# Performance work log

Hardware: AMD Instinct MI355X
Metric: run time of the kernel (lower is better)

## Reference

```python
import jax, jax.numpy as jnp
import numpy as np

N = 50000   # nodes per graph slot
E = 800000  # edges per graph slot
F = 768     # num_node_features
H = 256     # hidden_channels
G = 4       # max_graphs
B = 32      # graphs in batch
C1 = H * (G + 1)  # concat_channels = 1280


def setup_inputs() -> dict:
    key = jax.random.key(0)
    ks = iter(jax.random.split(key, 32))
    inp = {}
    for g in range(G):
        inp[f"x_g{g}"] = jax.random.normal(next(ks), (N, F), jnp.float32)
        inp[f"ei_g{g}"] = jax.random.randint(next(ks), (2, E), 0, N, jnp.int32)
        inp[f"batch_g{g}"] = jnp.sort(jax.random.randint(next(ks), (N,), 0, B, jnp.int32))
    inp["x_code"] = jax.random.normal(next(ks), (B, F), jnp.float32)
    s = 0.02
    inp["W1"] = jax.random.normal(next(ks), (F, H), jnp.float32) * s
    inp["b1"] = jnp.zeros((H,), jnp.float32)
    inp["W2"] = jax.random.normal(next(ks), (H, H), jnp.float32) * s
    inp["b2"] = jnp.zeros((H,), jnp.float32)
    inp["W3"] = jax.random.normal(next(ks), (H, H), jnp.float32) * s
    inp["b3"] = jnp.zeros((H,), jnp.float32)
    inp["Wc"] = jax.random.normal(next(ks), (F, H), jnp.float32) * s
    inp["bc"] = jnp.zeros((H,), jnp.float32)
    inp["Wl1"] = jax.random.normal(next(ks), (C1, C1 // 2), jnp.float32) * s
    inp["bl1"] = jnp.zeros((C1 // 2,), jnp.float32)
    inp["Wl2"] = jax.random.normal(next(ks), (C1 // 2, 2), jnp.float32) * s
    inp["bl2"] = jnp.zeros((2,), jnp.float32)
    return inp


def gcn_conv(x, W, b, src, dst):
    n = x.shape[0]
    h = x @ W                                   # [n, H]
    loops = jnp.arange(n, dtype=src.dtype)
    s = jnp.concatenate([src, loops])
    d = jnp.concatenate([dst, loops])
    deg = jax.ops.segment_sum(jnp.ones(s.shape[0], x.dtype), d, num_segments=n)
    dinv = jnp.where(deg > 0, jax.lax.rsqrt(deg), 0.0)
    norm = dinv[s] * dinv[d]                    # [E+n]
    return jax.ops.segment_sum(h[s] * norm[:, None], d, num_segments=n) + b


def global_mean_pool(x, batch, num_graphs):
    s = jax.ops.segment_sum(x, batch, num_segments=num_graphs)
    c = jax.ops.segment_sum(jnp.ones(x.shape[0], x.dtype), batch, num_segments=num_graphs)
    return s / jnp.maximum(c, 1.0)[:, None]


def reference(x_g0, x_g1, x_g2, x_g3, ei_g0, ei_g1, ei_g2, ei_g3,
              batch_g0, batch_g1, batch_g2, batch_g3, x_code,
              W1, b1, W2, b2, W3, b3, Wc, bc, Wl1, bl1, Wl2, bl2):
    nb = x_code.shape[0]
    pooled = []
    for x, ei, bi in zip((x_g0, x_g1, x_g2, x_g3),
                         (ei_g0, ei_g1, ei_g2, ei_g3),
                         (batch_g0, batch_g1, batch_g2, batch_g3)):
        h = jax.nn.relu(gcn_conv(x, W1, b1, ei[0], ei[1]))
        h = jax.nn.relu(gcn_conv(h, W2, b2, ei[0], ei[1]))
        h = gcn_conv(h, W3, b3, ei[0], ei[1])
        pooled.append(global_mean_pool(h, bi, nb))      # [B, H]
    xc = jax.nn.relu(x_code @ Wc + bc)                  # [B, H]
    pooled.append(xc)
    x_concat = jnp.concatenate(pooled, axis=1)          # [B, H*(G+1)]
    h = jax.nn.relu(x_concat @ Wl1 + bl1)
    # dropout p=0.2 with training=False -> identity
    logits = h @ Wl2 + bl2                              # [B, 2]
    return logits
```

## Files before the change

kernel.cpp:

```cpp
#include <hip/hip_runtime.h>
#include <hip/hip_bf16.h>

#define N_NODES 50000
#define N_EDGES 800000
#define F_IN    768
#define H_DIM   256
#define N_B     32
#define N_G     4
#define C1      1280
#define C2      640

typedef unsigned short u16;
typedef unsigned int u32;
typedef __bf16 bf16x8 __attribute__((ext_vector_type(8)));
typedef float f32x4 __attribute__((ext_vector_type(4)));

__device__ inline u16 f2b(float f) {
    u32 u = __builtin_bit_cast(u32, f);
    u += 0x7fffu + ((u >> 16) & 1u);
    return (u16)(u >> 16);
}
__device__ inline float b2f(u16 h) {
    u32 u = ((u32)h) << 16;
    return __builtin_bit_cast(float, u);
}
__device__ inline u32 pack2(float a, float b) {
    return (u32)f2b(a) | ((u32)f2b(b) << 16);
}


__global__ void count_deg_kernel(const int* __restrict__ dst, int* __restrict__ deg, int n_edges) {
    int e = blockIdx.x * blockDim.x + threadIdx.x;
    if (e < n_edges) atomicAdd(&deg[dst[e]], 1);
}

__global__ __launch_bounds__(1024) void scan1_kernel(const int* __restrict__ deg,
                                                     int* __restrict__ bsum, int n) {
    __shared__ int ws[16];
    int tid = threadIdx.x, lane = tid & 63, wid = tid >> 6;
    int i = blockIdx.x * 1024 + tid;
    int x = (i < n) ? deg[i] : 0;
#pragma unroll
    for (int off = 32; off; off >>= 1) x += __shfl_xor(x, off, 64);
    if (lane == 0) ws[wid] = x;
    __syncthreads();
    if (tid == 0) {
        int s = 0;
#pragma unroll
        for (int w = 0; w < 16; w++) s += ws[w];
        bsum[blockIdx.x] = s;
    }
}

__global__ __launch_bounds__(64) void scan2_kernel(int* __restrict__ bsum, int nb,
                                                   int* __restrict__ row_start, int n) {
    int lane = threadIdx.x;
    int x = (lane < nb) ? bsum[lane] : 0;
    int v = x;
#pragma unroll
    for (int off = 1; off < 64; off <<= 1) {
        int t = __shfl_up(v, off, 64);
        if (lane >= off) v += t;
    }
    if (lane < nb) bsum[lane] = v - x;
    if (lane == 63) row_start[n] = v;
}

__global__ __launch_bounds__(1024) void scan3_kernel(const int* __restrict__ deg,
                                                     const int* __restrict__ bsum,
                                                     int* __restrict__ row_start,
                                                     int* __restrict__ cursor,
                                                     float* __restrict__ dinv, int n) {
    __shared__ int ws[16];
    int tid = threadIdx.x, lane = tid & 63, wid = tid >> 6;
    int i = blockIdx.x * 1024 + tid;
    int x = (i < n) ? deg[i] : 0;
    int v = x;
#pragma unroll
    for (int off = 1; off < 64; off <<= 1) {
        int t = __shfl_up(v, off, 64);
        if (lane >= off) v += t;
    }
    if (lane == 63) ws[wid] = v;
    __syncthreads();
    if (wid == 0) {
        int s = (lane < 16) ? ws[lane] : 0;
#pragma unroll
        for (int off = 1; off < 16; off <<= 1) {
            int t = __shfl_up(s, off, 64);
            if (lane >= off) s += t;
        }
        if (lane < 16) ws[lane] = s;
    }
    __syncthreads();
    if (i < n) {
        int excl = bsum[blockIdx.x] + (wid ? ws[wid - 1] : 0) + (v - x);
        row_start[i] = excl;
        cursor[i] = excl;
        dinv[i] = rsqrtf((float)(x + 1));
    }
}

__global__ void fill_csr_kernel(const int* __restrict__ src, const int* __restrict__ dst,
                                int* __restrict__ cursor, int* __restrict__ csr_src, int n_edges) {
    int e = blockIdx.x * blockDim.x + threadIdx.x;
    if (e < n_edges) {
        int d = dst[e];
        int pos = atomicAdd(&cursor[d], 1);
        csr_src[pos] = src[e];
    }
}


__global__ void prep_w_kernel(const float* __restrict__ W, u16* __restrict__ Wt, int K) {
    int idx = blockIdx.x * blockDim.x + threadIdx.x;
    if (idx >= K * 256) return;
    int k = idx >> 8, n = idx & 255;
    Wt[(size_t)n * K + k] = f2b(W[idx]);
}


__global__ __launch_bounds__(256) void gemm_mfma_kernel(const void* __restrict__ Aptr, int a_fp32,
                                                        const u16* __restrict__ Wt,
                                                        const float* __restrict__ dinv,
                                                        u16* __restrict__ Cout, int n, int K) {
    __shared__ u16 As[64 * 32] __attribute__((aligned(16)));
    __shared__ u16 Bs[256 * 32] __attribute__((aligned(16)));
    int tid = threadIdx.x;
    int row0 = blockIdx.x * 64;
    int wid = tid >> 6, lane = tid & 63;
    int mlane = lane & 15, kg = lane >> 4;

    int ra = tid >> 2;
    int koffa = (tid & 3) << 3;
    int rga = row0 + ra; if (rga >= n) rga = n - 1;

    f32x4 acc[4][4];
#pragma unroll
    for (int a = 0; a < 4; a++)
#pragma unroll
        for (int b = 0; b < 4; b++)
#pragma unroll
            for (int c = 0; c < 4; c++) acc[a][b][c] = 0.f;

    for (int k0 = 0; k0 < K; k0 += 32) {
        if (a_fp32) {
            const float* A = (const float*)Aptr;
            const float* srcp = A + (size_t)rga * K + k0 + koffa;
            float4 f0 = *(const float4*)srcp;
            float4 f1 = *(const float4*)(srcp + 4);
            int4 v;
            v.x = (int)pack2(f0.x, f0.y);
            v.y = (int)pack2(f0.z, f0.w);
            v.z = (int)pack2(f1.x, f1.y);
            v.w = (int)pack2(f1.z, f1.w);
            *(int4*)&As[ra * 32 + koffa] = v;
        } else {
            const u16* A = (const u16*)Aptr;
            *(int4*)&As[ra * 32 + koffa] = *(const int4*)(A + (size_t)rga * K + k0 + koffa);
        }
#pragma unroll
        for (int it = 0; it < 4; it++) {
            int c = tid + it * 256;
            int r = c >> 2;
            int koff = (c & 3) << 3;
            *(int4*)&Bs[r * 32 + koff] = *(const int4*)(Wt + (size_t)r * K + k0 + koff);
        }
        __syncthreads();
        bf16x8 af[4], bfv[4];
#pragma unroll
        for (int mi = 0; mi < 4; mi++)
            af[mi] = *(const bf16x8*)&As[(mi * 16 + mlane) * 32 + kg * 8];
#pragma unroll
        for (int ni = 0; ni < 4; ni++)
            bfv[ni] = *(const bf16x8*)&Bs[(wid * 64 + ni * 16 + mlane) * 32 + kg * 8];
#pragma unroll
        for (int mi = 0; mi < 4; mi++)
#pragma unroll
            for (int ni = 0; ni < 4; ni++)
                acc[mi][ni] = __builtin_amdgcn_mfma_f32_16x16x32_bf16(af[mi], bfv[ni], acc[mi][ni], 0, 0, 0);
        __syncthreads();
    }
#pragma unroll
    for (int mi = 0; mi < 4; mi++) {
        int rbase = row0 + mi * 16 + kg * 4;
#pragma unroll
        for (int r = 0; r < 4; r++) {
            int row = rbase + r;
            if (row < n) {
                float s = dinv[row];
#pragma unroll
                for (int ni = 0; ni < 4; ni++) {
                    int col = wid * 64 + ni * 16 + mlane;
                    Cout[(size_t)row * H_DIM + col] = f2b(acc[mi][ni][r] * s);
                }
            }
        }
    }
}


__global__ __launch_bounds__(64) void aggregate_kernel(const u16* __restrict__ Ht,
                                                       const int* __restrict__ row_start,
                                                       const int* __restrict__ csr_src,
                                                       const float* __restrict__ dinv,
                                                       const float* __restrict__ bias,
                                                       u16* __restrict__ out, int do_relu) {
    int i = blockIdx.x;
    int c4 = threadIdx.x << 2;
    ushort4 sv = *(const ushort4*)(Ht + (size_t)i * H_DIM + c4);
    float a0 = b2f(sv.x), a1 = b2f(sv.y), a2 = b2f(sv.z), a3 = b2f(sv.w);
    int s = row_start[i], e = row_start[i + 1];
    for (int p = s; p < e; p++) {
        int j = csr_src[p];
        ushort4 v = *(const ushort4*)(Ht + (size_t)j * H_DIM + c4);
        a0 += b2f(v.x); a1 += b2f(v.y); a2 += b2f(v.z); a3 += b2f(v.w);
    }
    float di = dinv[i];
    float4 b = *(const float4*)(bias + c4);
    float o0 = a0 * di + b.x, o1 = a1 * di + b.y, o2 = a2 * di + b.z, o3 = a3 * di + b.w;
    if (do_relu) {
        o0 = fmaxf(o0, 0.f); o1 = fmaxf(o1, 0.f);
        o2 = fmaxf(o2, 0.f); o3 = fmaxf(o3, 0.f);
    }
    ushort4 ov = make_ushort4(f2b(o0), f2b(o1), f2b(o2), f2b(o3));
    *(ushort4*)(out + (size_t)i * H_DIM + c4) = ov;
}


__global__ __launch_bounds__(256) void pool_kernel(const u16* __restrict__ h3,
                                                   const int* __restrict__ batch,
                                                   float* __restrict__ concat, int g) {
    int tid = threadIdx.x;
    int per = (N_NODES + (int)gridDim.x - 1) / (int)gridDim.x;
    int start = blockIdx.x * per;
    int end = min(N_NODES, start + per);
    if (start >= end) return;
    float acc = 0.f;
    int cur = batch[start];
    for (int i = start; i < end; i++) {
        int b = batch[i];
        if (b != cur) {
            atomicAdd(&concat[cur * C1 + g * H_DIM + tid], acc);
            acc = 0.f;
            cur = b;
        }
        acc += b2f(h3[(size_t)i * H_DIM + tid]);
    }
    atomicAdd(&concat[cur * C1 + g * H_DIM + tid], acc);
}

__global__ __launch_bounds__(64) void count_kernel(const int* __restrict__ batch,
                                                   float* __restrict__ cnt, int g) {
    __shared__ int bound[N_B + 1];
    int t = threadIdx.x;
    if (t <= N_B) {
        int lo = 0, hi = N_NODES;
        while (lo < hi) {
            int mid = (lo + hi) >> 1;
            if (batch[mid] < t) lo = mid + 1; else hi = mid;
        }
        bound[t] = lo;
    }
    __syncthreads();
    if (t < N_B) cnt[g * N_B + t] = (float)(bound[t + 1] - bound[t]);
}

__global__ void pool_div_kernel(float* __restrict__ concat, const float* __restrict__ cnt) {
    int idx = blockIdx.x * blockDim.x + threadIdx.x;
    int g = idx >> 13;
    int r = idx & 8191;
    int b = r >> 8;
    int f = r & 255;
    float c = fmaxf(cnt[g * N_B + b], 1.f);
    concat[b * C1 + g * H_DIM + f] /= c;
}


__global__ void xc_kernel(const float* __restrict__ x_code, const float* __restrict__ Wc,
                          const float* __restrict__ bc, float* __restrict__ concat) {
    int idx = blockIdx.x * blockDim.x + threadIdx.x;
    int b = idx >> 8, c = idx & 255;
    float acc = bc[c];
    for (int k = 0; k < F_IN; k++) acc += x_code[b * F_IN + k] * Wc[k * H_DIM + c];
    concat[b * C1 + 4 * H_DIM + c] = fmaxf(acc, 0.f);
}

__global__ void mlp1_kernel(const float* __restrict__ concat, const float* __restrict__ Wl1,
                            const float* __restrict__ bl1, float* __restrict__ hmid) {
    int idx = blockIdx.x * blockDim.x + threadIdx.x;
    int b = idx / C2, c = idx % C2;
    float acc = bl1[c];
    for (int k = 0; k < C1; k++) acc += concat[b * C1 + k] * Wl1[k * C2 + c];
    hmid[b * C2 + c] = fmaxf(acc, 0.f);
}

__global__ void mlp2_kernel(const float* __restrict__ hmid, const float* __restrict__ Wl2,
                            const float* __restrict__ bl2, float* __restrict__ out) {
    int idx = threadIdx.x;
    if (idx < N_B * 2) {
        int b = idx >> 1, c = idx & 1;
        float acc = bl2[c];
        for (int k = 0; k < C2; k++) acc += hmid[b * C2 + k] * Wl2[k * 2 + c];
        out[b * 2 + c] = acc;
    }
}


extern "C" void kernel_launch(void* const* d_in, const int* in_sizes, int n_in,
                              void* d_out, int out_size, void* d_ws, size_t ws_size,
                              hipStream_t stream) {
    const float* x_g[N_G];
    const int* ei[N_G];
    const int* batch[N_G];
    for (int g = 0; g < N_G; g++) {
        x_g[g]   = (const float*)d_in[3 * g + 0];
        ei[g]    = (const int*)d_in[3 * g + 1];
        batch[g] = (const int*)d_in[3 * g + 2];
    }
    const float* x_code = (const float*)d_in[12];
    const float* W1 = (const float*)d_in[13];
    const float* b1 = (const float*)d_in[14];
    const float* W2 = (const float*)d_in[15];
    const float* b2 = (const float*)d_in[16];
    const float* W3 = (const float*)d_in[17];
    const float* b3 = (const float*)d_in[18];
    const float* Wc = (const float*)d_in[19];
    const float* bc = (const float*)d_in[20];
    const float* Wl1 = (const float*)d_in[21];
    const float* bl1 = (const float*)d_in[22];
    const float* Wl2 = (const float*)d_in[23];
    const float* bl2 = (const float*)d_in[24];
    float* out = (float*)d_out;

    char* p = (char*)d_ws;
    auto alloc = [&](size_t bytes) -> void* {
        void* q = (void*)p;
        p += (bytes + 255) & ~(size_t)255;
        return q;
    };
    u16*   bufA      = (u16*)alloc((size_t)N_NODES * H_DIM * 2);
    u16*   bufB      = (u16*)alloc((size_t)N_NODES * H_DIM * 2);
    u16*   Wt1       = (u16*)alloc((size_t)H_DIM * F_IN * 2);
    u16*   Wt2       = (u16*)alloc((size_t)H_DIM * H_DIM * 2);
    u16*   Wt3       = (u16*)alloc((size_t)H_DIM * H_DIM * 2);
    int*   row_start = (int*)alloc((size_t)(N_NODES + 1) * 4);
    int*   cursor    = (int*)alloc((size_t)N_NODES * 4);
    int*   csr_src   = (int*)alloc((size_t)N_EDGES * 4);
    int*   deg       = (int*)alloc((size_t)N_NODES * 4);
    float* dinv      = (float*)alloc((size_t)N_NODES * 4);
    float* concat    = (float*)alloc((size_t)N_B * C1 * 4);
    float* cnt       = (float*)alloc((size_t)N_G * N_B * 4);
    float* hmid      = (float*)alloc((size_t)N_B * C2 * 4);
    int*   bsum      = (int*)alloc((size_t)64 * 4);

    hipMemsetAsync(concat, 0, (size_t)N_B * C1 * 4, stream);

    prep_w_kernel<<<(F_IN * 256 + 255) / 256, 256, 0, stream>>>(W1, Wt1, F_IN);
    prep_w_kernel<<<(H_DIM * 256 + 255) / 256, 256, 0, stream>>>(W2, Wt2, H_DIM);
    prep_w_kernel<<<(H_DIM * 256 + 255) / 256, 256, 0, stream>>>(W3, Wt3, H_DIM);

    dim3 gemm_grid((N_NODES + 63) / 64);
    int nb_scan = (N_NODES + 1023) / 1024;

    for (int g = 0; g < N_G; g++) {
        const int* src = ei[g];
        const int* dst = ei[g] + N_EDGES;
        hipMemsetAsync(deg, 0, (size_t)N_NODES * 4, stream);
        count_deg_kernel<<<(N_EDGES + 255) / 256, 256, 0, stream>>>(dst, deg, N_EDGES);
        scan1_kernel<<<nb_scan, 1024, 0, stream>>>(deg, bsum, N_NODES);
        scan2_kernel<<<1, 64, 0, stream>>>(bsum, nb_scan, row_start, N_NODES);
        scan3_kernel<<<nb_scan, 1024, 0, stream>>>(deg, bsum, row_start, cursor, dinv, N_NODES);
        fill_csr_kernel<<<(N_EDGES + 255) / 256, 256, 0, stream>>>(src, dst, cursor, csr_src, N_EDGES);

        gemm_mfma_kernel<<<gemm_grid, 256, 0, stream>>>(x_g[g], 1, Wt1, dinv, bufA, N_NODES, F_IN);
        aggregate_kernel<<<N_NODES, 64, 0, stream>>>(bufA, row_start, csr_src, dinv, b1, bufB, 1);
        gemm_mfma_kernel<<<gemm_grid, 256, 0, stream>>>(bufB, 0, Wt2, dinv, bufA, N_NODES, H_DIM);
        aggregate_kernel<<<N_NODES, 64, 0, stream>>>(bufA, row_start, csr_src, dinv, b2, bufB, 1);
        gemm_mfma_kernel<<<gemm_grid, 256, 0, stream>>>(bufB, 0, Wt3, dinv, bufA, N_NODES, H_DIM);
        aggregate_kernel<<<N_NODES, 64, 0, stream>>>(bufA, row_start, csr_src, dinv, b3, bufB, 0);

        pool_kernel<<<2048, 256, 0, stream>>>(bufB, batch[g], concat, g);
        count_kernel<<<1, 64, 0, stream>>>(batch[g], cnt, g);
    }

    pool_div_kernel<<<(N_G * N_B * H_DIM) / 256, 256, 0, stream>>>(concat, cnt);
    xc_kernel<<<(N_B * H_DIM) / 256, 256, 0, stream>>>(x_code, Wc, bc, concat);
    mlp1_kernel<<<(N_B * C2) / 256, 256, 0, stream>>>(concat, Wl1, bl1, hmid);
    mlp2_kernel<<<1, 64, 0, stream>>>(hmid, Wl2, bl2, out);
}
```

Baseline: 2.277 ms.

## Double-buffer GEMM LDS tiles with register prefetch, pad LDS, batch aggregate nodes

The MFMA GEMM now stages A and B tiles through registers into double-buffered shared memory, so global loads for the next two k-steps overlap the MFMA work and one barrier per step is dropped. Shared-memory rows are padded to 40 elements to reduce bank conflicts on the fragment reads. The aggregation kernel handles four nodes per 256-thread block instead of one node per 64-thread block, which cuts block-launch overhead. Shared memory use per GEMM block roughly doubles, which may lower occupancy.

```diff
diff --git a/kernel.cpp b/kernel.cpp
--- a/kernel.cpp
+++ b/kernel.cpp
@@ -9,6 +9,7 @@
 #define N_G     4
 #define C1      1280
 #define C2      640
+#define LDA     40
 
 typedef unsigned short u16;
 typedef unsigned int u32;
@@ -124,8 +125,8 @@
                                                         const u16* __restrict__ Wt,
                                                         const float* __restrict__ dinv,
                                                         u16* __restrict__ Cout, int n, int K) {
-    __shared__ u16 As[64 * 32] __attribute__((aligned(16)));
-    __shared__ u16 Bs[256 * 32] __attribute__((aligned(16)));
+    __shared__ u16 As[2 * 64 * LDA] __attribute__((aligned(16)));
+    __shared__ u16 Bs[2 * 256 * LDA] __attribute__((aligned(16)));
     int tid = threadIdx.x;
     int row0 = blockIdx.x * 64;
     int wid = tid >> 6, lane = tid & 63;
@@ -134,6 +135,8 @@
     int ra = tid >> 2;
     int koffa = (tid & 3) << 3;
     int rga = row0 + ra; if (rga >= n) rga = n - 1;
+    const float* Af = (const float*)Aptr;
+    const u16*  Ab = (const u16*)Aptr;
 
     f32x4 acc[4][4];
 #pragma unroll
@@ -143,43 +146,64 @@
 #pragma unroll
             for (int c = 0; c < 4; c++) acc[a][b][c] = 0.f;
 
-    for (int k0 = 0; k0 < K; k0 += 32) {
+    int nk = K >> 5;
+    int4 stA, stB0, stB1, stB2, stB3;
+
+    auto loadA = [&](int k0, int4& d) {
         if (a_fp32) {
-            const float* A = (const float*)Aptr;
-            const float* srcp = A + (size_t)rga * K + k0 + koffa;
-            float4 f0 = *(const float4*)srcp;
-            float4 f1 = *(const float4*)(srcp + 4);
-            int4 v;
-            v.x = (int)pack2(f0.x, f0.y);
-            v.y = (int)pack2(f0.z, f0.w);
-            v.z = (int)pack2(f1.x, f1.y);
-            v.w = (int)pack2(f1.z, f1.w);
-            *(int4*)&As[ra * 32 + koffa] = v;
+            const float* s = Af + (size_t)rga * K + k0 + koffa;
+            float4 f0 = *(const float4*)s;
+            float4 f1 = *(const float4*)(s + 4);
+            d.x = (int)pack2(f0.x, f0.y);
+            d.y = (int)pack2(f0.z, f0.w);
+            d.z = (int)pack2(f1.x, f1.y);
+            d.w = (int)pack2(f1.z, f1.w);
         } else {
-            const u16* A = (const u16*)Aptr;
-            *(int4*)&As[ra * 32 + koffa] = *(const int4*)(A + (size_t)rga * K + k0 + koffa);
-        }
-#pragma unroll
-        for (int it = 0; it < 4; it++) {
-            int c = tid + it * 256;
-            int r = c >> 2;
-            int koff = (c & 3) << 3;
-            *(int4*)&Bs[r * 32 + koff] = *(const int4*)(Wt + (size_t)r * K + k0 + koff);
-        }
-        __syncthreads();
+            d = *(const int4*)(Ab + (size_t)rga * K + k0 + koffa);
+        }
+    };
+    auto loadB = [&](int k0) {
+        stB0 = *(const int4*)(Wt + (size_t)(ra +   0) * K + k0 + koffa);
+        stB1 = *(const int4*)(Wt + (size_t)(ra +  64) * K + k0 + koffa);
+        stB2 = *(const int4*)(Wt + (size_t)(ra + 128) * K + k0 + koffa);
+        stB3 = *(const int4*)(Wt + (size_t)(ra + 192) * K + k0 + koffa);
+    };
+    auto writeStage = [&](int buf) {
+        *(int4*)&As[buf * (64 * LDA) + ra * LDA + koffa] = stA;
+        u16* bb = &Bs[buf * (256 * LDA)];
+        *(int4*)&bb[(ra +   0) * LDA + koffa] = stB0;
+        *(int4*)&bb[(ra +  64) * LDA + koffa] = stB1;
+        *(int4*)&bb[(ra + 128) * LDA + koffa] = stB2;
+        *(int4*)&bb[(ra + 192) * LDA + koffa] = stB3;
+    };
+
+    loadA(0, stA); loadB(0);
+    writeStage(0);
+    if (nk > 1) { loadA(32, stA); loadB(32); }
+    __syncthreads();
+
+    int cur = 0;
+    for (int t = 0; t < nk; t++) {
+        const u16* ab = &As[cur * (64 * LDA)];
+        const u16* bb = &Bs[cur * (256 * LDA)];
         bf16x8 af[4], bfv[4];
 #pragma unroll
         for (int mi = 0; mi < 4; mi++)
-            af[mi] = *(const bf16x8*)&As[(mi * 16 + mlane) * 32 + kg * 8];
+            af[mi] = *(const bf16x8*)&ab[(mi * 16 + mlane) * LDA + kg * 8];
 #pragma unroll
         for (int ni = 0; ni < 4; ni++)
-            bfv[ni] = *(const bf16x8*)&Bs[(wid * 64 + ni * 16 + mlane) * 32 + kg * 8];
+            bfv[ni] = *(const bf16x8*)&bb[(wid * 64 + ni * 16 + mlane) * LDA + kg * 8];
+        if (t + 1 < nk) {
+            writeStage(cur ^ 1);
+            if (t + 2 < nk) { loadA((t + 2) << 5, stA); loadB((t + 2) << 5); }
+        }
 #pragma unroll
         for (int mi = 0; mi < 4; mi++)
 #pragma unroll
             for (int ni = 0; ni < 4; ni++)
                 acc[mi][ni] = __builtin_amdgcn_mfma_f32_16x16x32_bf16(af[mi], bfv[ni], acc[mi][ni], 0, 0, 0);
         __syncthreads();
+        cur ^= 1;
     }
 #pragma unroll
     for (int mi = 0; mi < 4; mi++) {
@@ -200,14 +224,15 @@
 }
 
 
-__global__ __launch_bounds__(64) void aggregate_kernel(const u16* __restrict__ Ht,
-                                                       const int* __restrict__ row_start,
-                                                       const int* __restrict__ csr_src,
-                                                       const float* __restrict__ dinv,
-                                                       const float* __restrict__ bias,
-                                                       u16* __restrict__ out, int do_relu) {
-    int i = blockIdx.x;
-    int c4 = threadIdx.x << 2;
+__global__ __launch_bounds__(256) void aggregate_kernel(const u16* __restrict__ Ht,
+                                                        const int* __restrict__ row_start,
+                                                        const int* __restrict__ csr_src,
+                                                        const float* __restrict__ dinv,
+                                                        const float* __restrict__ bias,
+                                                        u16* __restrict__ out, int do_relu) {
+    int i = blockIdx.x * 4 + (threadIdx.x >> 6);
+    if (i >= N_NODES) return;
+    int c4 = (threadIdx.x & 63) << 2;
     ushort4 sv = *(const ushort4*)(Ht + (size_t)i * H_DIM + c4);
     float a0 = b2f(sv.x), a1 = b2f(sv.y), a2 = b2f(sv.z), a3 = b2f(sv.w);
     int s = row_start[i], e = row_start[i + 1];
@@ -361,6 +386,7 @@
     prep_w_kernel<<<(H_DIM * 256 + 255) / 256, 256, 0, stream>>>(W3, Wt3, H_DIM);
 
     dim3 gemm_grid((N_NODES + 63) / 64);
+    dim3 agg_grid((N_NODES + 3) / 4);
     int nb_scan = (N_NODES + 1023) / 1024;
 
     for (int g = 0; g < N_G; g++) {
@@ -374,11 +400,11 @@
         fill_csr_kernel<<<(N_EDGES + 255) / 256, 256, 0, stream>>>(src, dst, cursor, csr_src, N_EDGES);
 
         gemm_mfma_kernel<<<gemm_grid, 256, 0, stream>>>(x_g[g], 1, Wt1, dinv, bufA, N_NODES, F_IN);
-        aggregate_kernel<<<N_NODES, 64, 0, stream>>>(bufA, row_start, csr_src, dinv, b1, bufB, 1);
+        aggregate_kernel<<<agg_grid, 256, 0, stream>>>(bufA, row_start, csr_src, dinv, b1, bufB, 1);
         gemm_mfma_kernel<<<gemm_grid, 256, 0, stream>>>(bufB, 0, Wt2, dinv, bufA, N_NODES, H_DIM);
-        aggregate_kernel<<<N_NODES, 64, 0, stream>>>(bufA, row_start, csr_src, dinv, b2, bufB, 1);
+        aggregate_kernel<<<agg_grid, 256, 0, stream>>>(bufA, row_start, csr_src, dinv, b2, bufB, 1);
         gemm_mfma_kernel<<<gemm_grid, 256, 0, stream>>>(bufB, 0, Wt3, dinv, bufA, N_NODES, H_DIM);
-        aggregate_kernel<<<N_NODES, 64, 0, stream>>>(bufA, row_start, csr_src, dinv, b3, bufB, 0);
+        aggregate_kernel<<<agg_grid, 256, 0, stream>>>(bufA, row_start, csr_src, dinv, b3, bufB, 0);
 
         pool_kernel<<<2048, 256, 0, stream>>>(bufB, batch[g], concat, g);
         count_kernel<<<1, 64, 0, stream>>>(batch[g], cnt, g);
```

Result: slower. 2.556 ms (+12.3%).

## Software-pipeline GEMM with double-buffered LDS, direct B register loads, swizzle

Applied to the files above, without the earlier changes.

Rewrites the node-feature GEMM as a template on K and input type, so the inner loop is specialised at compile time. The A tile is double-buffered in LDS with an XOR swizzle to cut bank conflicts. Global loads for the next K-step are issued before the current step's MFMAs, overlapping memory latency with compute. The weight operand is loaded straight from global memory into registers, skipping LDS staging. In exchange, register pressure rises and each wave re-reads the weights from cache instead of sharing them through LDS.

```diff
diff --git a/kernel.cpp b/kernel.cpp
--- a/kernel.cpp
+++ b/kernel.cpp
@@ -120,20 +120,26 @@
 }
 
 
-__global__ __launch_bounds__(256) void gemm_mfma_kernel(const void* __restrict__ Aptr, int a_fp32,
+template<int K, bool AFP32>
+__global__ __launch_bounds__(256) void gemm_mfma_kernel(const void* __restrict__ Aptr,
                                                         const u16* __restrict__ Wt,
                                                         const float* __restrict__ dinv,
-                                                        u16* __restrict__ Cout, int n, int K) {
-    __shared__ u16 As[64 * 32] __attribute__((aligned(16)));
-    __shared__ u16 Bs[256 * 32] __attribute__((aligned(16)));
+                                                        u16* __restrict__ Cout, int n) {
+    constexpr int NK = K / 32;
+    __shared__ u16 As[2 * 2048] __attribute__((aligned(16)));
     int tid = threadIdx.x;
     int row0 = blockIdx.x * 64;
     int wid = tid >> 6, lane = tid & 63;
     int mlane = lane & 15, kg = lane >> 4;
 
     int ra = tid >> 2;
-    int koffa = (tid & 3) << 3;
+    int qa = tid & 3;
     int rga = row0 + ra; if (rga >= n) rga = n - 1;
+    const float* Af = (const float*)Aptr;
+    const u16*  Ab = (const u16*)Aptr;
+    int awr = (ra * 32 + qa * 8) ^ (((ra >> 1) & 3) << 3);
+
+    const u16* wtb = Wt + (size_t)(wid * 64 + mlane) * K + kg * 8;
 
     f32x4 acc[4][4];
 #pragma unroll
@@ -143,44 +149,69 @@
 #pragma unroll
             for (int c = 0; c < 4; c++) acc[a][b][c] = 0.f;
 
-    for (int k0 = 0; k0 < K; k0 += 32) {
-        if (a_fp32) {
-            const float* A = (const float*)Aptr;
-            const float* srcp = A + (size_t)rga * K + k0 + koffa;
-            float4 f0 = *(const float4*)srcp;
-            float4 f1 = *(const float4*)(srcp + 4);
-            int4 v;
-            v.x = (int)pack2(f0.x, f0.y);
-            v.y = (int)pack2(f0.z, f0.w);
-            v.z = (int)pack2(f1.x, f1.y);
-            v.w = (int)pack2(f1.z, f1.w);
-            *(int4*)&As[ra * 32 + koffa] = v;
+    float4 rF0, rF1; int4 rA;
+    auto loadA = [&](int s) {
+        int k0 = (s < NK ? s : NK - 1) * 32;
+        if constexpr (AFP32) {
+            const float* sp = Af + (size_t)rga * K + k0 + qa * 8;
+            rF0 = *(const float4*)sp;
+            rF1 = *(const float4*)(sp + 4);
         } else {
-            const u16* A = (const u16*)Aptr;
-            *(int4*)&As[ra * 32 + koffa] = *(const int4*)(A + (size_t)rga * K + k0 + koffa);
-        }
-#pragma unroll
-        for (int it = 0; it < 4; it++) {
-            int c = tid + it * 256;
-            int r = c >> 2;
-            int koff = (c & 3) << 3;
-            *(int4*)&Bs[r * 32 + koff] = *(const int4*)(Wt + (size_t)r * K + k0 + koff);
-        }
+            rA = *(const int4*)(Ab + (size_t)rga * K + k0 + qa * 8);
+        }
+    };
+    auto writeA = [&](int buf) {
+        int4 v;
+        if constexpr (AFP32) {
+            v.x = (int)pack2(rF0.x, rF0.y); v.y = (int)pack2(rF0.z, rF0.w);
+            v.z = (int)pack2(rF1.x, rF1.y); v.w = (int)pack2(rF1.z, rF1.w);
+        } else {
+            v = rA;
+        }
+        *(int4*)&As[buf * 2048 + awr] = v;
+    };
+    auto loadB = [&](bf16x8* b, int s) {
+        int k0 = (s < NK ? s : NK - 1) * 32;
+#pragma unroll
+        for (int ni = 0; ni < 4; ni++)
+            b[ni] = *(const bf16x8*)(wtb + (size_t)ni * 16 * K + k0);
+    };
+    auto readA = [&](bf16x8* a, int buf) {
+#pragma unroll
+        for (int mi = 0; mi < 4; mi++) {
+            int m = mi * 16 + mlane;
+            a[mi] = *(const bf16x8*)&As[buf * 2048 + ((m * 32 + kg * 8) ^ (((m >> 1) & 3) << 3))];
+        }
+    };
+    auto domfma = [&](bf16x8* a, bf16x8* b) {
+#pragma unroll
+        for (int mi = 0; mi < 4; mi++)
+#pragma unroll
+            for (int ni = 0; ni < 4; ni++)
+                acc[mi][ni] = __builtin_amdgcn_mfma_f32_16x16x32_bf16(a[mi], b[ni], acc[mi][ni], 0, 0, 0);
+    };
+
+    bf16x8 b0[4], b1[4], af[4];
+    loadA(0); writeA(0);
+    loadA(1);
+    loadB(b0, 0);
+    __syncthreads();
+
+    for (int t = 0; t < NK; t += 2) {
+        readA(af, 0);
+        writeA(1);
+        loadA(t + 2);
+        loadB(b1, t + 1);
+        domfma(af, b0);
         __syncthreads();
-        bf16x8 af[4], bfv[4];
-#pragma unroll
-        for (int mi = 0; mi < 4; mi++)
-            af[mi] = *(const bf16x8*)&As[(mi * 16 + mlane) * 32 + kg * 8];
-#pragma unroll
-        for (int ni = 0; ni < 4; ni++)
-            bfv[ni] = *(const bf16x8*)&Bs[(wid * 64 + ni * 16 + mlane) * 32 + kg * 8];
-#pragma unroll
-        for (int mi = 0; mi < 4; mi++)
-#pragma unroll
-            for (int ni = 0; ni < 4; ni++)
-                acc[mi][ni] = __builtin_amdgcn_mfma_f32_16x16x32_bf16(af[mi], bfv[ni], acc[mi][ni], 0, 0, 0);
+        readA(af, 1);
+        writeA(0);
+        loadA(t + 3);
+        loadB(b0, t + 2);
+        domfma(af, b1);
         __syncthreads();
     }
+
 #pragma unroll
     for (int mi = 0; mi < 4; mi++) {
         int rbase = row0 + mi * 16 + kg * 4;
@@ -373,11 +404,11 @@
         scan3_kernel<<<nb_scan, 1024, 0, stream>>>(deg, bsum, row_start, cursor, dinv, N_NODES);
         fill_csr_kernel<<<(N_EDGES + 255) / 256, 256, 0, stream>>>(src, dst, cursor, csr_src, N_EDGES);
 
-        gemm_mfma_kernel<<<gemm_grid, 256, 0, stream>>>(x_g[g], 1, Wt1, dinv, bufA, N_NODES, F_IN);
+        gemm_mfma_kernel<F_IN, true><<<gemm_grid, 256, 0, stream>>>(x_g[g], Wt1, dinv, bufA, N_NODES);
         aggregate_kernel<<<N_NODES, 64, 0, stream>>>(bufA, row_start, csr_src, dinv, b1, bufB, 1);
-        gemm_mfma_kernel<<<gemm_grid, 256, 0, stream>>>(bufB, 0, Wt2, dinv, bufA, N_NODES, H_DIM);
+        gemm_mfma_kernel<H_DIM, false><<<gemm_grid, 256, 0, stream>>>(bufB, Wt2, dinv, bufA, N_NODES);
         aggregate_kernel<<<N_NODES, 64, 0, stream>>>(bufA, row_start, csr_src, dinv, b2, bufB, 1);
-        gemm_mfma_kernel<<<gemm_grid, 256, 0, stream>>>(bufB, 0, Wt3, dinv, bufA, N_NODES, H_DIM);
+        gemm_mfma_kernel<H_DIM, false><<<gemm_grid, 256, 0, stream>>>(bufB, Wt3, dinv, bufA, N_NODES);
         aggregate_kernel<<<N_NODES, 64, 0, stream>>>(bufA, row_start, csr_src, dinv, b3, bufB, 0);
 
         pool_kernel<<<2048, 256, 0, stream>>>(bufB, batch[g], concat, g);
```

Measured after the change: 2.286 ms. Within noise of the previous version (+0.4%).
